# Kernel optimization log

Hardware: AMD Instinct MI355X
Metric: run time of the kernel (lower is better)

## Reference

```python
import jax, jax.numpy as jnp
import numpy as np

EMBED_DIM = 2048
NUM_HEADS = 16
HEAD_DIM = EMBED_DIM // NUM_HEADS
SCALE = EMBED_DIM ** -0.5  # NOTE: original uses full embed_dim, not head_dim


def setup_inputs() -> dict:
    key = jax.random.key(0)
    ks = jax.random.split(key, 9)
    d = EMBED_DIM
    s = 1.0 / np.sqrt(d)
    inp = {
        "x": jax.random.normal(ks[0], (2, 2048, d), dtype=jnp.float32),
        "wq": jax.random.uniform(ks[1], (d, d), jnp.float32, -s, s),
        "bq": jnp.zeros((d,), jnp.float32),
        "wk": jax.random.uniform(ks[2], (d, d), jnp.float32, -s, s),
        "bk": jnp.zeros((d,), jnp.float32),
        "wv": jax.random.uniform(ks[3], (d, d), jnp.float32, -s, s),
        "bv": jnp.zeros((d,), jnp.float32),
        "wo": jax.random.uniform(ks[4], (d, d), jnp.float32, -s, s),
        "bo": jnp.zeros((d,), jnp.float32),
    }
    return inp


def reference(x, wq, bq, wk, bk, wv, bv, wo, bo):
    b, t, d = x.shape
    h, hd = NUM_HEADS, HEAD_DIM
    # projections (torch Linear: x @ W.T + b; here weights stored as [in, out])
    q = (x @ wq + bq).reshape(b, t, h, hd).transpose(0, 2, 1, 3)  # [b,h,t,hd]
    k = (x @ wk + bk).reshape(b, t, h, hd).transpose(0, 2, 1, 3)
    v = (x @ wv + bv).reshape(b, t, h, hd).transpose(0, 2, 1, 3)
    scores = jnp.einsum("bhqd,bhkd->bhqk", q, k) * SCALE
    probs = jax.nn.softmax(scores, axis=-1)
    attn = jnp.einsum("bhqk,bhkd->bhqd", probs, v)
    attn = attn.transpose(0, 2, 1, 3).reshape(b, t, d)
    return attn @ wo + bo
```

## Files before the change

kernel.cpp:

```cpp
#include <hip/hip_runtime.h>

typedef unsigned int u32;
typedef __bf16 bf16;
typedef bf16 bf16x2 __attribute__((ext_vector_type(2)));
typedef bf16 bf16x4 __attribute__((ext_vector_type(4)));
typedef bf16 bf16x8 __attribute__((ext_vector_type(8)));
typedef float f32x4 __attribute__((ext_vector_type(4)));
typedef float f32x16 __attribute__((ext_vector_type(16)));
typedef u32 u32x4 __attribute__((ext_vector_type(4)));

#define T_ 2048
#define D_ 2048
#define H_ 16
#define HD_ 128
#define SCALE_ 0.022097086912079608f
#define LOG2E_ 1.4426950408889634f

typedef __attribute__((address_space(1))) u32 gu32;
typedef __attribute__((address_space(3))) u32 lu32;

__device__ __forceinline__ void gload_lds16(const void* g, void* l) {
  __builtin_amdgcn_global_load_lds((gu32*)(void*)g, (lu32*)l, 16, 0, 0);
}

__device__ __forceinline__ u32 packbf(float a, float b) {
  union { bf16x2 v; u32 u; } c;
  c.v.x = (bf16)a; c.v.y = (bf16)b;
  return c.u;
}

__global__ void cast_x_kernel(const float* __restrict__ x, bf16* __restrict__ xb) {
  int i = blockIdx.x * 256 + threadIdx.x;
  float4 v = ((const float4*)x)[i];
  bf16x4 o;
  o.x = (bf16)v.x; o.y = (bf16)v.y; o.z = (bf16)v.z; o.w = (bf16)v.w;
  ((bf16x4*)xb)[i] = o;
}

__global__ void twcast_kernel(const float* __restrict__ w0, const float* __restrict__ w1,
                              const float* __restrict__ w2, const float* __restrict__ w3,
                              bf16* __restrict__ o0, bf16* __restrict__ o1,
                              bf16* __restrict__ o2, bf16* __restrict__ o3) {
  int z = blockIdx.z;
  const float* W = (z == 0) ? w0 : (z == 1) ? w1 : (z == 2) ? w2 : w3;
  bf16* O = (z == 0) ? o0 : (z == 1) ? o1 : (z == 2) ? o2 : o3;
  __shared__ float tile[64][65];
  int t = threadIdx.x, tx = t & 15, ty = t >> 4;
  int n0 = blockIdx.x * 64, k0 = blockIdx.y * 64;
#pragma unroll
  for (int i = 0; i < 4; i++) {
    float4 v = *(const float4*)&W[(size_t)(k0 + ty + i * 16) * D_ + n0 + tx * 4];
    tile[ty + i * 16][tx * 4 + 0] = v.x;
    tile[ty + i * 16][tx * 4 + 1] = v.y;
    tile[ty + i * 16][tx * 4 + 2] = v.z;
    tile[ty + i * 16][tx * 4 + 3] = v.w;
  }
  __syncthreads();
#pragma unroll
  for (int i = 0; i < 4; i++) {
    int n = ty + i * 16;
    bf16x4 o;
    o.x = (bf16)tile[tx * 4 + 0][n];
    o.y = (bf16)tile[tx * 4 + 1][n];
    o.z = (bf16)tile[tx * 4 + 2][n];
    o.w = (bf16)tile[tx * 4 + 3][n];
    *(bf16x4*)&O[(size_t)(n0 + n) * D_ + k0 + tx * 4] = o;
  }
}

__device__ __forceinline__ void stage_tile(const bf16* __restrict__ A,
                                           const bf16* __restrict__ Bt,
                                           char* aT, char* bT,
                                           int m0, int n0, int k0, int t) {
#pragma unroll
  for (int i = 0; i < 4; i++) {
    int L = i * 4096 + t * 16;
    int row = L >> 7;
    int kb = (L & 127) ^ ((row & 7) << 4);
    gload_lds16(A + (size_t)(m0 + row) * 2048 + k0 + (kb >> 1), aT + L);
    gload_lds16(Bt + (size_t)(n0 + row) * 2048 + k0 + (kb >> 1), bT + L);
  }
}

__device__ __forceinline__ void gemm_compute64(const char* aT, const char* bT,
                                               f32x4 acc[4][4], int lane, int wr, int wc) {
#pragma unroll
  for (int kk = 0; kk < 2; kk++) {
    int ak = kk * 64 + ((lane >> 4) << 4);
    bf16x8 af[4], bfv[4];
#pragma unroll
    for (int f = 0; f < 4; f++) {
      int ar = wr * 64 + f * 16 + (lane & 15);
      af[f] = *(const bf16x8*)(aT + ar * 128 + (ak ^ ((ar & 7) << 4)));
      int br = wc * 64 + f * 16 + (lane & 15);
      bfv[f] = *(const bf16x8*)(bT + br * 128 + (ak ^ ((br & 7) << 4)));
    }
#pragma unroll
    for (int mi = 0; mi < 4; mi++)
#pragma unroll
      for (int ni = 0; ni < 4; ni++)
        acc[mi][ni] = __builtin_amdgcn_mfma_f32_16x16x32_bf16(af[mi], bfv[ni], acc[mi][ni], 0, 0, 0);
  }
}

__device__ __forceinline__ void gemm_core_128(const bf16* __restrict__ A,
                                              const bf16* __restrict__ Bt,
                                              f32x4 acc[4][4], int m0, int n0) {
  __shared__ char smem[65536];
  const int t = threadIdx.x;
  const int lane = t & 63;
  const int wr = (t >> 7) & 1;
  const int wc = (t >> 6) & 1;
  stage_tile(A, Bt, smem, smem + 16384, m0, n0, 0, t);
  __syncthreads();
  int cur = 0;
  for (int k0 = 64; k0 < 2048; k0 += 64) {
    char* base = smem + (cur ^ 1) * 32768;
    stage_tile(A, Bt, base, base + 16384, m0, n0, k0, t);
    char* cbase = smem + cur * 32768;
    gemm_compute64(cbase, cbase + 16384, acc, lane, wr, wc);
    __syncthreads();
    cur ^= 1;
  }
  char* cbase = smem + cur * 32768;
  gemm_compute64(cbase, cbase + 16384, acc, lane, wr, wc);
}

__global__ __launch_bounds__(256, 2) void qkv_gemm_kernel(
    const bf16* __restrict__ xb,
    const bf16* __restrict__ wqt, const bf16* __restrict__ wkt, const bf16* __restrict__ wvt,
    const float* __restrict__ bq, const float* __restrict__ bk, const float* __restrict__ bv,
    bf16* __restrict__ Qb, bf16* __restrict__ Kb, bf16* __restrict__ Vtb) {
  const bf16* Bt; const float* bias; float scale;
  int z = blockIdx.z;
  if (z == 0)      { Bt = wqt; bias = bq; scale = SCALE_ * LOG2E_; }
  else if (z == 1) { Bt = wkt; bias = bk; scale = 1.0f; }
  else             { Bt = wvt; bias = bv; scale = 1.0f; }
  int m0 = blockIdx.y * 128, n0 = blockIdx.x * 128;
  f32x4 zero = {0.f, 0.f, 0.f, 0.f};
  f32x4 acc[4][4];
#pragma unroll
  for (int mi = 0; mi < 4; mi++)
#pragma unroll
    for (int ni = 0; ni < 4; ni++) acc[mi][ni] = zero;
  gemm_core_128(xb, Bt, acc, m0, n0);
  int lane = threadIdx.x & 63;
  int wr = (threadIdx.x >> 7) & 1, wc = (threadIdx.x >> 6) & 1;
  if (z < 2) {
    bf16* Out = (z == 0) ? Qb : Kb;
#pragma unroll
    for (int ni = 0; ni < 4; ni++) {
      int cn = n0 + wc * 64 + ni * 16 + (lane & 15);
      float bb = bias[cn];
      int h = cn >> 7, hd = cn & 127;
#pragma unroll
      for (int mi = 0; mi < 4; mi++) {
        int rm = m0 + wr * 64 + mi * 16 + ((lane >> 4) << 2);
#pragma unroll
        for (int r = 0; r < 4; r++) {
          int mg = rm + r;
          int b = mg >> 11, tt = mg & 2047;
          Out[(size_t)((b * H_ + h) * T_ + tt) * HD_ + hd] = (bf16)((acc[mi][ni][r] + bb) * scale);
        }
      }
    }
  } else {
#pragma unroll
    for (int ni = 0; ni < 4; ni++) {
      int cn = n0 + wc * 64 + ni * 16 + (lane & 15);
      float bb = bias[cn];
      int h = cn >> 7, hd = cn & 127;
#pragma unroll
      for (int mi = 0; mi < 4; mi++) {
        int rm = m0 + wr * 64 + mi * 16 + ((lane >> 4) << 2);
        int b = rm >> 11, tt = rm & 2047;
        bf16x4 st;
        st.x = (bf16)(acc[mi][ni][0] + bb);
        st.y = (bf16)(acc[mi][ni][1] + bb);
        st.z = (bf16)(acc[mi][ni][2] + bb);
        st.w = (bf16)(acc[mi][ni][3] + bb);
        *(bf16x4*)&Vtb[((size_t)(b * H_ + h) * HD_ + hd) * T_ + tt] = st;
      }
    }
  }
}

__global__ __launch_bounds__(256, 2) void attn_kernel(
    const bf16* __restrict__ Qb, const bf16* __restrict__ Kb,
    const bf16* __restrict__ Vtb, bf16* __restrict__ Ab) {
  __shared__ char smem[65536];
  const int t = threadIdx.x, lane = t & 63, w = t >> 6;
  const int h0 = lane >> 5;
  const int q = lane & 31;
  int bid = blockIdx.x;
  int wid = (bid & 7) * 64 + (bid >> 3);
  const int bh = wid >> 4;
  const int q0 = (wid & 15) * 128;
  const bf16* Qh = Qb + (size_t)bh * T_ * HD_;
  const bf16* Kh = Kb + (size_t)bh * T_ * HD_;
  const bf16* Vh = Vtb + (size_t)bh * HD_ * T_;

  bf16x8 qf[8];
  {
    const bf16* qrow = Qh + (size_t)(q0 + w * 32 + q) * HD_ + h0 * 8;
#pragma unroll
    for (int kf = 0; kf < 8; kf++) qf[kf] = *(const bf16x8*)(qrow + kf * 16);
  }

  f32x16 o[4];
#pragma unroll
  for (int nb = 0; nb < 4; nb++)
#pragma unroll
    for (int r = 0; r < 16; r++) o[nb][r] = 0.f;
  float m = -1e30f, l = 0.f;

  auto stage = [&](int kt, char* Kl, char* Vl) {
#pragma unroll
    for (int i = 0; i < 4; i++) {
      int L = i * 4096 + t * 16;
      int rowK = L >> 8;
      int kbK = (L & 255) ^ ((rowK & 7) << 4);
      gload_lds16(Kh + (size_t)(kt + rowK) * HD_ + (kbK >> 1), Kl + L);
      int rowV = L >> 7;
      int kbV = (L & 127) ^ ((rowV & 7) << 4);
      gload_lds16(Vh + (size_t)rowV * T_ + kt + (kbV >> 1), Vl + L);
    }
  };

  stage(0, smem, smem + 16384);
  __syncthreads();
  int cur = 0;

  for (int kt = 0; kt < T_; kt += 64) {
    char* Klds = smem + cur * 32768;
    char* Vlds = Klds + 16384;
    if (kt + 64 < T_) {
      char* nxt = smem + (cur ^ 1) * 32768;
      stage(kt + 64, nxt, nxt + 16384);
    }

    f32x16 s[2];
#pragma unroll
    for (int sub = 0; sub < 2; sub++)
#pragma unroll
      for (int r = 0; r < 16; r++) s[sub][r] = 0.f;
#pragma unroll
    for (int kf = 0; kf < 8; kf++) {
#pragma unroll
      for (int sub = 0; sub < 2; sub++) {
        int rr = sub * 32 + q;
        bf16x8 kfr = *(const bf16x8*)(Klds + rr * 256 + ((kf * 32 + h0 * 16) ^ ((rr & 7) << 4)));
        s[sub] = __builtin_amdgcn_mfma_f32_32x32x16_bf16(kfr, qf[kf], s[sub], 0, 0, 0);
      }
    }

    float mx = s[0][0];
#pragma unroll
    for (int sub = 0; sub < 2; sub++)
#pragma unroll
      for (int r = 0; r < 16; r++) mx = fmaxf(mx, s[sub][r]);
    mx = fmaxf(mx, __shfl_xor(mx, 32));
    if (__any(mx > m + 8.f)) {
      float mn = fmaxf(m, mx);
      float fac = exp2f(m - mn);
      m = mn;
      l *= fac;
#pragma unroll
      for (int nb = 0; nb < 4; nb++)
#pragma unroll
        for (int r = 0; r < 16; r++) o[nb][r] *= fac;
    }
    float rs = 0.f;
#pragma unroll
    for (int sub = 0; sub < 2; sub++)
#pragma unroll
      for (int r = 0; r < 16; r++) {
        float p = exp2f(s[sub][r] - m);
        s[sub][r] = p;
        rs += p;
      }
    rs += __shfl_xor(rs, 32);
    l += rs;

    bf16x8 pfrag[4];
#pragma unroll
    for (int sub = 0; sub < 2; sub++) {
#pragma unroll
      for (int c = 0; c < 2; c++) {
        u32 X0 = packbf(s[sub][8 * c + 0], s[sub][8 * c + 1]);
        u32 X1 = packbf(s[sub][8 * c + 2], s[sub][8 * c + 3]);
        u32 Y0 = packbf(s[sub][8 * c + 4], s[sub][8 * c + 5]);
        u32 Y1 = packbf(s[sub][8 * c + 6], s[sub][8 * c + 7]);
        u32 sX0 = (u32)__shfl_xor((int)X0, 32);
        u32 sX1 = (u32)__shfl_xor((int)X1, 32);
        u32 sY0 = (u32)__shfl_xor((int)Y0, 32);
        u32 sY1 = (u32)__shfl_xor((int)Y1, 32);
        u32x4 wv;
        wv.x = h0 ? sY0 : X0;
        wv.y = h0 ? sY1 : X1;
        wv.z = h0 ? Y0 : sX0;
        wv.w = h0 ? Y1 : sX1;
        union { u32x4 u; bf16x8 b; } cv;
        cv.u = wv;
        pfrag[sub * 2 + c] = cv.b;
      }
    }

#pragma unroll
    for (int nb = 0; nb < 4; nb++) {
      int vr = nb * 32 + q;
#pragma unroll
      for (int ks = 0; ks < 4; ks++) {
        bf16x8 vf = *(const bf16x8*)(Vlds + vr * 128 + ((ks * 32 + h0 * 16) ^ ((vr & 7) << 4)));
        o[nb] = __builtin_amdgcn_mfma_f32_32x32x16_bf16(vf, pfrag[ks], o[nb], 0, 0, 0);
      }
    }
    __syncthreads();
    cur ^= 1;
  }

  float inv = 1.f / l;
  int b = bh >> 4, hh = bh & 15;
  bf16* orow = Ab + ((size_t)b * T_ + q0 + w * 32 + q) * D_ + hh * HD_;
#pragma unroll
  for (int nb = 0; nb < 4; nb++)
#pragma unroll
    for (int g = 0; g < 4; g++) {
      bf16x4 st;
      st.x = (bf16)(o[nb][4 * g + 0] * inv);
      st.y = (bf16)(o[nb][4 * g + 1] * inv);
      st.z = (bf16)(o[nb][4 * g + 2] * inv);
      st.w = (bf16)(o[nb][4 * g + 3] * inv);
      *(bf16x4*)(orow + nb * 32 + 8 * g + 4 * h0) = st;
    }
}

__global__ __launch_bounds__(256, 2) void out_gemm_kernel(
    const bf16* __restrict__ Ab, const bf16* __restrict__ wot,
    const float* __restrict__ bo, float* __restrict__ out) {
  int m0 = blockIdx.y * 128, n0 = blockIdx.x * 128;
  f32x4 zero = {0.f, 0.f, 0.f, 0.f};
  f32x4 acc[4][4];
#pragma unroll
  for (int mi = 0; mi < 4; mi++)
#pragma unroll
    for (int ni = 0; ni < 4; ni++) acc[mi][ni] = zero;
  gemm_core_128(Ab, wot, acc, m0, n0);
  int lane = threadIdx.x & 63;
  int wr = (threadIdx.x >> 7) & 1, wc = (threadIdx.x >> 6) & 1;
#pragma unroll
  for (int ni = 0; ni < 4; ni++) {
    int cn = n0 + wc * 64 + ni * 16 + (lane & 15);
    float bb = bo[cn];
#pragma unroll
    for (int mi = 0; mi < 4; mi++) {
      int rm = m0 + wr * 64 + mi * 16 + ((lane >> 4) << 2);
#pragma unroll
      for (int r = 0; r < 4; r++)
        out[(size_t)(rm + r) * D_ + cn] = acc[mi][ni][r] + bb;
    }
  }
}

extern "C" void kernel_launch(void* const* d_in, const int* in_sizes, int n_in,
                              void* d_out, int out_size, void* d_ws, size_t ws_size,
                              hipStream_t stream) {
  const float* x  = (const float*)d_in[0];
  const float* wq = (const float*)d_in[1];
  const float* bq = (const float*)d_in[2];
  const float* wk = (const float*)d_in[3];
  const float* bk = (const float*)d_in[4];
  const float* wv = (const float*)d_in[5];
  const float* bv = (const float*)d_in[6];
  const float* wo = (const float*)d_in[7];
  const float* bo = (const float*)d_in[8];
  float* out = (float*)d_out;
  char* ws = (char*)d_ws;

  bf16* xb  = (bf16*)(ws);
  bf16* wqt = (bf16*)(ws + 16777216);
  bf16* wkt = (bf16*)(ws + 25165824);
  bf16* wvt = (bf16*)(ws + 33554432);
  bf16* wot = (bf16*)(ws + 41943040);
  bf16* Qb  = (bf16*)(ws + 50331648);
  bf16* Kb  = (bf16*)(ws + 67108864);
  bf16* Vtb = (bf16*)(ws + 83886080);
  bf16* Ab  = xb;

  cast_x_kernel<<<8192, 256, 0, stream>>>(x, xb);
  twcast_kernel<<<dim3(32, 32, 4), 256, 0, stream>>>(wq, wk, wv, wo, wqt, wkt, wvt, wot);
  qkv_gemm_kernel<<<dim3(16, 32, 3), 256, 0, stream>>>(xb, wqt, wkt, wvt, bq, bk, bv, Qb, Kb, Vtb);
  attn_kernel<<<512, 256, 0, stream>>>(Qb, Kb, Vtb, Ab);
  out_gemm_kernel<<<dim3(16, 32), 256, 0, stream>>>(Ab, wot, bo, out);

  (void)in_sizes; (void)n_in; (void)out_size; (void)ws_size;
}
```

Before: 397.4 us.

## Merge cast kernels, remap GEMM block order for XCDs, tune attention inner loop

Folds the x cast into the weight-transpose kernel as an extra grid slice, which removes one launch. Both GEMMs now remap the block index so that consecutive tiles land on the same XCD, aiming for better L2 reuse of shared A and B tiles. In the attention kernel the LDS swizzle offsets are precomputed, s_setprio is raised around the MFMA sections, and the row max becomes a pairwise reduction tree. These are several separate tweaks to scheduling and cache locality, none of which changes the algorithm.

```diff
diff --git a/kernel.cpp b/kernel.cpp
--- a/kernel.cpp
+++ b/kernel.cpp
@@ -29,23 +29,29 @@
   return c.u;
 }
 
-__global__ void cast_x_kernel(const float* __restrict__ x, bf16* __restrict__ xb) {
-  int i = blockIdx.x * 256 + threadIdx.x;
-  float4 v = ((const float4*)x)[i];
-  bf16x4 o;
-  o.x = (bf16)v.x; o.y = (bf16)v.y; o.z = (bf16)v.z; o.w = (bf16)v.w;
-  ((bf16x4*)xb)[i] = o;
-}
-
-__global__ void twcast_kernel(const float* __restrict__ w0, const float* __restrict__ w1,
-                              const float* __restrict__ w2, const float* __restrict__ w3,
-                              bf16* __restrict__ o0, bf16* __restrict__ o1,
-                              bf16* __restrict__ o2, bf16* __restrict__ o3) {
+__global__ void prep_kernel(const float* __restrict__ x, bf16* __restrict__ xb,
+                            const float* __restrict__ w0, const float* __restrict__ w1,
+                            const float* __restrict__ w2, const float* __restrict__ w3,
+                            bf16* __restrict__ o0, bf16* __restrict__ o1,
+                            bf16* __restrict__ o2, bf16* __restrict__ o3) {
   int z = blockIdx.z;
+  int t = threadIdx.x;
+  if (z == 4) {
+    int b2 = blockIdx.y * 32 + blockIdx.x;
+#pragma unroll
+    for (int j = 0; j < 8; j++) {
+      int i = b2 * 2048 + j * 256 + t;
+      float4 v = ((const float4*)x)[i];
+      bf16x4 o;
+      o.x = (bf16)v.x; o.y = (bf16)v.y; o.z = (bf16)v.z; o.w = (bf16)v.w;
+      ((bf16x4*)xb)[i] = o;
+    }
+    return;
+  }
   const float* W = (z == 0) ? w0 : (z == 1) ? w1 : (z == 2) ? w2 : w3;
   bf16* O = (z == 0) ? o0 : (z == 1) ? o1 : (z == 2) ? o2 : o3;
   __shared__ float tile[64][65];
-  int t = threadIdx.x, tx = t & 15, ty = t >> 4;
+  int tx = t & 15, ty = t >> 4;
   int n0 = blockIdx.x * 64, k0 = blockIdx.y * 64;
 #pragma unroll
   for (int i = 0; i < 4; i++) {
@@ -136,7 +142,9 @@
   if (z == 0)      { Bt = wqt; bias = bq; scale = SCALE_ * LOG2E_; }
   else if (z == 1) { Bt = wkt; bias = bk; scale = 1.0f; }
   else             { Bt = wvt; bias = bv; scale = 1.0f; }
-  int m0 = blockIdx.y * 128, n0 = blockIdx.x * 128;
+  int bid = blockIdx.x;
+  int wid = (bid & 7) * 64 + (bid >> 3);
+  int n0 = (wid & 15) * 128, m0 = (wid >> 4) * 128;
   f32x4 zero = {0.f, 0.f, 0.f, 0.f};
   f32x4 acc[4][4];
 #pragma unroll
@@ -200,6 +208,12 @@
   const bf16* Kh = Kb + (size_t)bh * T_ * HD_;
   const bf16* Vh = Vtb + (size_t)bh * HD_ * T_;
 
+  int soff[8];
+#pragma unroll
+  for (int kf = 0; kf < 8; kf++) soff[kf] = (kf * 32 + h0 * 16) ^ ((q & 7) << 4);
+  const int kbase = q * 256;
+  const int vbase = q * 128;
+
   bf16x8 qf[8];
   {
     const bf16* qrow = Qh + (size_t)(q0 + w * 32 + q) * HD_ + h0 * 8;
@@ -232,8 +246,8 @@
   int cur = 0;
 
   for (int kt = 0; kt < T_; kt += 64) {
-    char* Klds = smem + cur * 32768;
-    char* Vlds = Klds + 16384;
+    const char* Klds = smem + cur * 32768;
+    const char* Vlds = Klds + 16384;
     if (kt + 64 < T_) {
       char* nxt = smem + (cur ^ 1) * 32768;
       stage(kt + 64, nxt, nxt + 16384);
@@ -244,21 +258,23 @@
     for (int sub = 0; sub < 2; sub++)
 #pragma unroll
       for (int r = 0; r < 16; r++) s[sub][r] = 0.f;
+    __builtin_amdgcn_s_setprio(1);
 #pragma unroll
     for (int kf = 0; kf < 8; kf++) {
 #pragma unroll
       for (int sub = 0; sub < 2; sub++) {
-        int rr = sub * 32 + q;
-        bf16x8 kfr = *(const bf16x8*)(Klds + rr * 256 + ((kf * 32 + h0 * 16) ^ ((rr & 7) << 4)));
+        bf16x8 kfr = *(const bf16x8*)(Klds + kbase + sub * 8192 + soff[kf]);
         s[sub] = __builtin_amdgcn_mfma_f32_32x32x16_bf16(kfr, qf[kf], s[sub], 0, 0, 0);
       }
     }
-
-    float mx = s[0][0];
+    __builtin_amdgcn_s_setprio(0);
+
+    float mx = fmaxf(s[0][0], s[0][1]);
 #pragma unroll
     for (int sub = 0; sub < 2; sub++)
 #pragma unroll
-      for (int r = 0; r < 16; r++) mx = fmaxf(mx, s[sub][r]);
+      for (int r = (sub == 0 ? 2 : 0); r < 16; r += 2)
+        mx = fmaxf(mx, fmaxf(s[sub][r], s[sub][r + 1]));
     mx = fmaxf(mx, __shfl_xor(mx, 32));
     if (__any(mx > m + 8.f)) {
       float mn = fmaxf(m, mx);
@@ -306,15 +322,16 @@
       }
     }
 
+    __builtin_amdgcn_s_setprio(1);
 #pragma unroll
     for (int nb = 0; nb < 4; nb++) {
-      int vr = nb * 32 + q;
 #pragma unroll
       for (int ks = 0; ks < 4; ks++) {
-        bf16x8 vf = *(const bf16x8*)(Vlds + vr * 128 + ((ks * 32 + h0 * 16) ^ ((vr & 7) << 4)));
+        bf16x8 vf = *(const bf16x8*)(Vlds + vbase + nb * 4096 + soff[ks]);
         o[nb] = __builtin_amdgcn_mfma_f32_32x32x16_bf16(vf, pfrag[ks], o[nb], 0, 0, 0);
       }
     }
+    __builtin_amdgcn_s_setprio(0);
     __syncthreads();
     cur ^= 1;
   }
@@ -338,7 +355,9 @@
 __global__ __launch_bounds__(256, 2) void out_gemm_kernel(
     const bf16* __restrict__ Ab, const bf16* __restrict__ wot,
     const float* __restrict__ bo, float* __restrict__ out) {
-  int m0 = blockIdx.y * 128, n0 = blockIdx.x * 128;
+  int bid = blockIdx.x;
+  int wid = (bid & 7) * 64 + (bid >> 3);
+  int n0 = (wid & 15) * 128, m0 = (wid >> 4) * 128;
   f32x4 zero = {0.f, 0.f, 0.f, 0.f};
   f32x4 acc[4][4];
 #pragma unroll
@@ -387,11 +406,10 @@
   bf16* Vtb = (bf16*)(ws + 83886080);
   bf16* Ab  = xb;
 
-  cast_x_kernel<<<8192, 256, 0, stream>>>(x, xb);
-  twcast_kernel<<<dim3(32, 32, 4), 256, 0, stream>>>(wq, wk, wv, wo, wqt, wkt, wvt, wot);
-  qkv_gemm_kernel<<<dim3(16, 32, 3), 256, 0, stream>>>(xb, wqt, wkt, wvt, bq, bk, bv, Qb, Kb, Vtb);
+  prep_kernel<<<dim3(32, 32, 5), 256, 0, stream>>>(x, xb, wq, wk, wv, wo, wqt, wkt, wvt, wot);
+  qkv_gemm_kernel<<<dim3(512, 1, 3), 256, 0, stream>>>(xb, wqt, wkt, wvt, bq, bk, bv, Qb, Kb, Vtb);
   attn_kernel<<<512, 256, 0, stream>>>(Qb, Kb, Vtb, Ab);
-  out_gemm_kernel<<<dim3(16, 32), 256, 0, stream>>>(Ab, wot, bo, out);
+  out_gemm_kernel<<<512, 256, 0, stream>>>(Ab, wot, bo, out);
 
   (void)in_sizes; (void)n_in; (void)out_size; (void)ws_size;
 }
```

Result: faster. 384.5 us (-3.2%).
